# Kernel tuning notes

Hardware: AMD Instinct MI355X
Metric: run time of the kernel (lower is better)

The kernel has to match this reference:

```python
import jax, jax.numpy as jnp
import numpy as np

# MLA dims (DeepSeek-V3-lite style)
B, S, DIM = 1, 2048, 2048
H, NOPE, ROPE, VD, LORA = 16, 128, 64, 128, 512
QK_HEAD = NOPE + ROPE  # 192
SCALE = QK_HEAD ** -0.5
EPS = 1e-6


def _rmsnorm(x, w):
    return x * jax.lax.rsqrt(jnp.mean(x * x, axis=-1, keepdims=True) + EPS) * w


def _apply_rope(x, cos, sin):
    # x: [b, s, h, d] with interleaved (real, imag) pairs; cos/sin: [s, d//2]
    x0, x1 = x[..., 0::2], x[..., 1::2]
    c = cos[None, :, None, :]
    s = sin[None, :, None, :]
    y0 = x0 * c - x1 * s
    y1 = x0 * s + x1 * c
    return jnp.stack([y0, y1], axis=-1).reshape(x.shape)


def setup_inputs() -> dict:
    key = jax.random.key(0)
    ks = jax.random.split(key, 6)
    x = jax.random.normal(ks[0], (B, S, DIM), jnp.float32) * 0.02
    wq = jax.random.normal(ks[1], (H * QK_HEAD, DIM), jnp.float32) * 0.02
    wkv_a = jax.random.normal(ks[2], (LORA + ROPE, DIM), jnp.float32) * 0.02
    kv_norm_w = jnp.ones((LORA,), jnp.float32)
    wkv_b = jax.random.normal(ks[3], (H * (NOPE + VD), LORA), jnp.float32) * 0.02
    wo = jax.random.normal(ks[4], (DIM, H * VD), jnp.float32) * 0.02
    # rotary freqs_cis (cos/sin) for qk_rope_head_dim
    inv_freq = 1.0 / (10000.0 ** (np.arange(0, ROPE, 2, dtype=np.float32) / ROPE))
    t = np.arange(S, dtype=np.float32)
    ang = np.outer(t, inv_freq)  # [S, ROPE//2]
    cos = jnp.asarray(np.cos(ang), jnp.float32)
    sin = jnp.asarray(np.sin(ang), jnp.float32)
    return {"x": x, "cos": cos, "sin": sin, "wq": wq, "wkv_a": wkv_a,
            "kv_norm_w": kv_norm_w, "wkv_b": wkv_b, "wo": wo}


def reference(x, cos, sin, wq, wkv_a, kv_norm_w, wkv_b, wo):
    b, s, _ = x.shape
    # queries
    q = (x @ wq.T).reshape(b, s, H, QK_HEAD)
    q_nope, q_pe = q[..., :NOPE], q[..., NOPE:]
    q_pe = _apply_rope(q_pe, cos, sin)  # [b,s,h,rope]
    # latent kv
    kv = x @ wkv_a.T  # [b,s,lora+rope]
    kv_c, k_pe = kv[..., :LORA], kv[..., LORA:]
    k_pe = _apply_rope(k_pe[:, :, None, :], cos, sin)[:, :, 0, :]  # [b,s,rope]
    kv_c = _rmsnorm(kv_c, kv_norm_w)  # latent kv cache [b,s,lora]
    # absorbed weights: wkv_b viewed as [h, nope+vd, lora]
    wkv_b_r = wkv_b.reshape(H, NOPE + VD, LORA)
    w_uk = wkv_b_r[:, :NOPE]   # [h, nope, lora]
    w_uv = wkv_b_r[:, NOPE:]   # [h, vd, lora]
    # absorb: project q_nope into latent space
    q_c = jnp.einsum('bshd,hdc->bshc', q_nope, w_uk)  # [b,s,h,lora]
    scores = (jnp.einsum('bshc,btc->bsht', q_c, kv_c)
              + jnp.einsum('bshr,btr->bsht', q_pe, k_pe)) * SCALE
    # causal mask over [s, t]
    mask = jnp.where(jnp.arange(s)[:, None] >= jnp.arange(s)[None, :], 0.0, -1e30)
    scores = scores + mask[None, :, None, :].astype(scores.dtype)
    attn = jax.nn.softmax(scores, axis=-1)
    o = jnp.einsum('bsht,btc->bshc', attn, kv_c)       # [b,s,h,lora]
    o = jnp.einsum('bshc,hdc->bshd', o, w_uv)           # [b,s,h,vd]
    out = o.reshape(b, s, H * VD) @ wo.T                # [b,s,dim]
    return out
```

## Files before the change

### kernel.cpp

```cpp
#include <hip/hip_runtime.h>
#include <hip/hip_bf16.h>
#include <math.h>

#define S_LEN 2048
#define DIM   2048
#define H_N   16
#define NOPE  128
#define ROPE  64
#define VD    128
#define LORA  512
#define D_QK  576
#define SCALE_F 0.07216878364870323f
#define EPS_F 1e-6f
#define KVF 640
#define KVS 1280

typedef short short8 __attribute__((ext_vector_type(8)));
typedef short short4v __attribute__((ext_vector_type(4)));
typedef float floatx4 __attribute__((ext_vector_type(4)));

static __device__ inline unsigned short f2bf_bits(float f) {
  union { __hip_bfloat16 h; unsigned short u; } cv;
  cv.h = __float2bfloat16(f);
  return cv.u;
}

static __device__ inline float bf2f(unsigned short b) {
  union { unsigned u; float f; } cv;
  cv.u = (unsigned)b << 16;
  return cv.f;
}

static __device__ inline void gload_lds16(const short* gptr, short* lds_base_uniform) {
  __builtin_amdgcn_global_load_lds(
      (const __attribute__((address_space(1))) void*)gptr,
      (__attribute__((address_space(3))) void*)lds_base_uniform, 16, 0, 0);
}

static __device__ inline void cast8(const float* __restrict__ src,
                                    short* __restrict__ dst, int i) {
  float4 a = ((const float4*)src)[2 * i];
  float4 b = ((const float4*)src)[2 * i + 1];
  uint4 o;
  o.x = (unsigned)f2bf_bits(a.x) | ((unsigned)f2bf_bits(a.y) << 16);
  o.y = (unsigned)f2bf_bits(a.z) | ((unsigned)f2bf_bits(a.w) << 16);
  o.z = (unsigned)f2bf_bits(b.x) | ((unsigned)f2bf_bits(b.y) << 16);
  o.w = (unsigned)f2bf_bits(b.z) | ((unsigned)f2bf_bits(b.w) << 16);
  ((uint4*)dst)[i] = o;
}

#define CSEG0 524288
#define CSEG1 (CSEG0 + 786432)
#define CSEG2 (CSEG1 + 147456)
#define CSEG3 (CSEG2 + 16384)
#define CSEG4 (CSEG3 + 262144)
#define CSEG5 (CSEG4 + 524288)
__global__ __launch_bounds__(256) void cast_all(
    const float* __restrict__ x, const float* __restrict__ wq,
    const float* __restrict__ wkv_a, const float* __restrict__ wkv_b,
    const float* __restrict__ wo, short* __restrict__ xb,
    short* __restrict__ wcat, short* __restrict__ wkvbb,
    short* __restrict__ wob) {
  int i = blockIdx.x * 256 + threadIdx.x;
  if (i < CSEG0) {
    cast8(x, xb, i);
  } else if (i < CSEG1) {
    cast8(wq, wcat, i - CSEG0);
  } else if (i < CSEG2) {
    cast8(wkv_a, wcat + 3072 * 2048, i - CSEG1);
  } else if (i < CSEG3) {
    ((uint4*)(wcat + 3072 * 2048 + 576 * 2048))[i - CSEG2] = (uint4){0u, 0u, 0u, 0u};
  } else if (i < CSEG4) {
    cast8(wkv_b, wkvbb, i - CSEG3);
  } else if (i < CSEG5) {
    cast8(wo, wob, i - CSEG4);
  }
}

__global__ __launch_bounds__(256) void transpose_wuk(
    const float* __restrict__ wkvb, short* __restrict__ wukT) {
  __shared__ float tile[32][33];
  const int h = blockIdx.z, c0 = blockIdx.y * 32, d0 = blockIdx.x * 32;
  const int t = threadIdx.x;
  const int r = t >> 3, c4 = (t & 7) * 4;
  float4 v = *(const float4*)(wkvb + ((long)h * 256 + d0 + r) * 512 + c0 + c4);
  tile[r][c4 + 0] = v.x; tile[r][c4 + 1] = v.y;
  tile[r][c4 + 2] = v.z; tile[r][c4 + 3] = v.w;
  __syncthreads();
  uint2 o;
  o.x = (unsigned)f2bf_bits(tile[c4 + 0][r]) | ((unsigned)f2bf_bits(tile[c4 + 1][r]) << 16);
  o.y = (unsigned)f2bf_bits(tile[c4 + 2][r]) | ((unsigned)f2bf_bits(tile[c4 + 3][r]) << 16);
  *(uint2*)(wukT + ((long)h * 512 + c0 + r) * 128 + d0 + c4) = o;
}

__global__ __launch_bounds__(256) void gemm_bf16_nt_m64(
    const short* __restrict__ A, const short* __restrict__ B, void* __restrict__ Cv,
    int K, int lda, int ldb, int ldc, long aB, long bB, long cB, int bf16out) {
  A += (long)blockIdx.z * aB;
  B += (long)blockIdx.z * bB;
  const int m0 = blockIdx.y * 64, n0 = blockIdx.x * 128;
  __shared__ short As[2][64 * 32];
  __shared__ short Bs[2][128 * 32];
  const int tid = threadIdx.x, w = tid >> 6, lane = tid & 63;
  const int ln = lane & 15, g = lane >> 4;
  const int mw = (w & 1) * 32, nw = (w >> 1) * 64;
  floatx4 acc[2][4];
#pragma unroll
  for (int i = 0; i < 2; ++i)
#pragma unroll
    for (int j = 0; j < 4; ++j) acc[i][j] = (floatx4){0.f, 0.f, 0.f, 0.f};

#define GEMM_STAGE64(k0_, b_)                                                  \
  {                                                                            \
    {                                                                          \
      const int bc = w * 64;                                                   \
      const int c = bc + lane;                                                 \
      const int row = c >> 2, quar = c & 3;                                    \
      gload_lds16(A + (long)(m0 + row) * lda + (k0_) + quar * 8, As[b_] + bc * 8); \
    }                                                                          \
    _Pragma("unroll")                                                          \
    for (int i = 0; i < 2; ++i) {                                              \
      const int bc = (i * 4 + w) * 64;                                         \
      const int c = bc + lane;                                                 \
      const int row = c >> 2, quar = c & 3;                                    \
      gload_lds16(B + (long)(n0 + row) * ldb + (k0_) + quar * 8, Bs[b_] + bc * 8); \
    }                                                                          \
  }

  GEMM_STAGE64(0, 0);
  __syncthreads();
  const int nk = K >> 5;
  for (int kt = 0; kt < nk; ++kt) {
    const int cb = kt & 1;
    if (kt + 1 < nk) GEMM_STAGE64((kt + 1) << 5, cb ^ 1);
    short8 af[2], bf_[4];
#pragma unroll
    for (int mi = 0; mi < 2; ++mi)
      af[mi] = *(const short8*)(As[cb] + (mw + mi * 16 + ln) * 32 + g * 8);
#pragma unroll
    for (int ni = 0; ni < 4; ++ni)
      bf_[ni] = *(const short8*)(Bs[cb] + (nw + ni * 16 + ln) * 32 + g * 8);
#pragma unroll
    for (int mi = 0; mi < 2; ++mi)
#pragma unroll
      for (int ni = 0; ni < 4; ++ni)
        acc[mi][ni] = __builtin_amdgcn_mfma_f32_16x16x32_bf16(af[mi], bf_[ni], acc[mi][ni], 0, 0, 0);
    __syncthreads();
  }
#undef GEMM_STAGE64
  if (bf16out) {
    short* Cs = (short*)Cv + (long)blockIdx.z * cB;
#pragma unroll
    for (int mi = 0; mi < 2; ++mi)
#pragma unroll
      for (int ni = 0; ni < 4; ++ni)
#pragma unroll
        for (int r = 0; r < 4; ++r)
          Cs[(long)(m0 + mw + mi * 16 + g * 4 + r) * ldc + n0 + nw + ni * 16 + ln] =
              (short)f2bf_bits(acc[mi][ni][r]);
  } else {
    float* C = (float*)Cv + (long)blockIdx.z * cB;
#pragma unroll
    for (int mi = 0; mi < 2; ++mi)
#pragma unroll
      for (int ni = 0; ni < 4; ++ni)
#pragma unroll
        for (int r = 0; r < 4; ++r)
          C[(long)(m0 + mw + mi * 16 + g * 4 + r) * ldc + n0 + nw + ni * 16 + ln] = acc[mi][ni][r];
  }
}

__global__ __launch_bounds__(256) void gemm_qkv_m64(
    const short* __restrict__ A, const short* __restrict__ B,
    short* __restrict__ Cq, float* __restrict__ Ckv) {
  const int m0 = blockIdx.y * 64, n0 = blockIdx.x * 128;
  __shared__ short As[2][64 * 32];
  __shared__ short Bs[2][128 * 32];
  const int tid = threadIdx.x, w = tid >> 6, lane = tid & 63;
  const int ln = lane & 15, g = lane >> 4;
  const int mw = (w & 1) * 32, nw = (w >> 1) * 64;
  floatx4 acc[2][4];
#pragma unroll
  for (int i = 0; i < 2; ++i)
#pragma unroll
    for (int j = 0; j < 4; ++j) acc[i][j] = (floatx4){0.f, 0.f, 0.f, 0.f};

#define QKV_STAGE(k0_, b_)                                                     \
  {                                                                            \
    {                                                                          \
      const int bc = w * 64;                                                   \
      const int c = bc + lane;                                                 \
      const int row = c >> 2, quar = c & 3;                                    \
      gload_lds16(A + (long)(m0 + row) * 2048 + (k0_) + quar * 8, As[b_] + bc * 8); \
    }                                                                          \
    _Pragma("unroll")                                                          \
    for (int i = 0; i < 2; ++i) {                                              \
      const int bc = (i * 4 + w) * 64;                                         \
      const int c = bc + lane;                                                 \
      const int row = c >> 2, quar = c & 3;                                    \
      gload_lds16(B + (long)(n0 + row) * 2048 + (k0_) + quar * 8, Bs[b_] + bc * 8); \
    }                                                                          \
  }

  QKV_STAGE(0, 0);
  __syncthreads();
  for (int kt = 0; kt < 64; ++kt) {
    const int cb = kt & 1;
    if (kt + 1 < 64) QKV_STAGE((kt + 1) << 5, cb ^ 1);
    short8 af[2], bf_[4];
#pragma unroll
    for (int mi = 0; mi < 2; ++mi)
      af[mi] = *(const short8*)(As[cb] + (mw + mi * 16 + ln) * 32 + g * 8);
#pragma unroll
    for (int ni = 0; ni < 4; ++ni)
      bf_[ni] = *(const short8*)(Bs[cb] + (nw + ni * 16 + ln) * 32 + g * 8);
#pragma unroll
    for (int mi = 0; mi < 2; ++mi)
#pragma unroll
      for (int ni = 0; ni < 4; ++ni)
        acc[mi][ni] = __builtin_amdgcn_mfma_f32_16x16x32_bf16(af[mi], bf_[ni], acc[mi][ni], 0, 0, 0);
    __syncthreads();
  }
#undef QKV_STAGE
  if (n0 < 3072) {
#pragma unroll
    for (int mi = 0; mi < 2; ++mi)
#pragma unroll
      for (int ni = 0; ni < 4; ++ni)
#pragma unroll
        for (int r = 0; r < 4; ++r)
          Cq[(long)(m0 + mw + mi * 16 + g * 4 + r) * 3072 + n0 + nw + ni * 16 + ln] =
              (short)f2bf_bits(acc[mi][ni][r]);
  } else {
#pragma unroll
    for (int mi = 0; mi < 2; ++mi)
#pragma unroll
      for (int ni = 0; ni < 4; ++ni)
#pragma unroll
        for (int r = 0; r < 4; ++r)
          Ckv[(long)(m0 + mw + mi * 16 + g * 4 + r) * KVF + (n0 - 3072) + nw + ni * 16 + ln] =
              acc[mi][ni][r];
  }
}

__global__ __launch_bounds__(64) void prep_kernel(
    float* kv, const short* __restrict__ qbufb, short* __restrict__ qhatb,
    const float* __restrict__ cosp, const float* __restrict__ sinp,
    const float* __restrict__ normw) {
  const int s = blockIdx.x;
  const int l = threadIdx.x;
  float* row = kv + (long)s * KVF;
  short* krow = (short*)kv + (long)s * KVS;

  float4 v0 = *(const float4*)(row + l * 8);
  float4 v1 = *(const float4*)(row + l * 8 + 4);
  float rx0 = 0.f, rx1 = 0.f, rc = 0.f, rs = 0.f;
  if (l < 32) {
    rc = cosp[s * 32 + l];
    rs = sinp[s * 32 + l];
    rx0 = row[512 + 2 * l];
    rx1 = row[512 + 2 * l + 1];
  }
  float4 w0 = *(const float4*)(normw + l * 8);
  float4 w1 = *(const float4*)(normw + l * 8 + 4);

  float ss = v0.x * v0.x + v0.y * v0.y + v0.z * v0.z + v0.w * v0.w +
             v1.x * v1.x + v1.y * v1.y + v1.z * v1.z + v1.w * v1.w;
#pragma unroll
  for (int off = 32; off; off >>= 1) ss += __shfl_xor(ss, off, 64);
  const float scale = rsqrtf(ss * (1.0f / (float)LORA) + EPS_F);
  v0.x *= scale * w0.x; v0.y *= scale * w0.y; v0.z *= scale * w0.z; v0.w *= scale * w0.w;
  v1.x *= scale * w1.x; v1.y *= scale * w1.y; v1.z *= scale * w1.z; v1.w *= scale * w1.w;

  uint4 pk;
  pk.x = (unsigned)f2bf_bits(v0.x) | ((unsigned)f2bf_bits(v0.y) << 16);
  pk.y = (unsigned)f2bf_bits(v0.z) | ((unsigned)f2bf_bits(v0.w) << 16);
  pk.z = (unsigned)f2bf_bits(v1.x) | ((unsigned)f2bf_bits(v1.y) << 16);
  pk.w = (unsigned)f2bf_bits(v1.z) | ((unsigned)f2bf_bits(v1.w) << 16);
  *(uint4*)(krow + l * 8) = pk;

  if (l < 32) {
    const float y0 = rx0 * rc - rx1 * rs;
    const float y1 = rx0 * rs + rx1 * rc;
    unsigned pr = (unsigned)f2bf_bits(y0) | ((unsigned)f2bf_bits(y1) << 16);
    *(unsigned*)(krow + 512 + 2 * l) = pr;
  }

#pragma unroll
  for (int it = 0; it < 8; ++it) {
    const int p = it * 64 + l;
    const int h = p >> 5;
    const int i = p & 31;
    const float c = cosp[s * 32 + i];
    const float sn = sinp[s * 32 + i];
    const short* qp = qbufb + (long)s * 3072 + h * 192 + NOPE;
    const unsigned uq = *(const unsigned*)(qp + 2 * i);
    const float x0 = bf2f((unsigned short)uq);
    const float x1 = bf2f((unsigned short)(uq >> 16));
    const float y0 = x0 * c - x1 * sn;
    const float y1 = x0 * sn + x1 * c;
    short* dst = qhatb + ((long)h * S_LEN + s) * D_QK + 512;
    *(unsigned*)(dst + 2 * i) = (unsigned)f2bf_bits(y0) | ((unsigned)f2bf_bits(y1) << 16);
  }
}

__global__ __launch_bounds__(256) void transpose_v(
    const short* __restrict__ kbf, short* __restrict__ kvt) {
  __shared__ short tile[32][36];
  const int d0 = blockIdx.x * 32;
  const int s0 = blockIdx.y * 32;
  const int t = threadIdx.x;
  const int r = t >> 3;
  const int c4 = (t & 7) * 4;
  uint2 v = *(const uint2*)(kbf + (long)(s0 + r) * KVS + d0 + c4);
  *(uint2*)(&tile[r][c4]) = v;
  __syncthreads();
  uint2 o;
  o.x = (unsigned)(unsigned short)tile[c4 + 0][r] | ((unsigned)(unsigned short)tile[c4 + 1][r] << 16);
  o.y = (unsigned)(unsigned short)tile[c4 + 2][r] | ((unsigned)(unsigned short)tile[c4 + 3][r] << 16);
  *(uint2*)(kvt + (long)(d0 + r) * S_LEN + s0 + c4) = o;
}

__global__ __launch_bounds__(256) void build_ktt(
    const short* __restrict__ kbf, short* __restrict__ ktt) {
  const int kt = blockIdx.x;
  for (int idx = threadIdx.x; idx < 18 * 64; idx += 256) {
    const int c = idx >> 6, l = idx & 63;
    const int ln = l & 15, g = l >> 4;
    uint4 v = *(const uint4*)(kbf + (long)(kt * 16 + ln) * KVS + c * 32 + g * 8);
    *(uint4*)(ktt + ((long)(kt * 18 + c) * 64 + l) * 8) = v;
  }
}

__global__ __launch_bounds__(256) void build_vtt(
    const short* __restrict__ kvt, short* __restrict__ vtt) {
  const int kt = blockIdx.x;
  for (int idx = threadIdx.x; idx < 32 * 64; idx += 256) {
    const int nt = idx >> 6, l = idx & 63;
    const int ln = l & 15, g = l >> 4;
    uint4 v = *(const uint4*)(kvt + (long)(nt * 16 + ln) * S_LEN + kt * 32 + g * 8);
    *(uint4*)(vtt + ((long)(kt * 32 + nt) * 64 + l) * 8) = v;
  }
}

__global__ __launch_bounds__(512, 2) void flash_reg(
    const short* __restrict__ qhat,
    const short* __restrict__ ktt,
    const short* __restrict__ vtt,
    short* __restrict__ obuf) {
  const int bid = blockIdx.x;
  const int hp = bid & 7;
  const int v = bid >> 3;
  const int vi = v & 31, vj = v >> 5;
  const int qt2 = (vj == 0) ? 63 - vi : vi;
  const int q0 = qt2 * 32;
  const int tid = threadIdx.x;
  const int w = tid >> 6;
  const int lane = tid & 63;
  const int ln = lane & 15, g = lane >> 4;
  const int hh = w & 1;
  const int dh = (w >> 1) & 1;
  const int qt = w >> 2;
  const int h = hp * 2 + hh;
  const int qrow = q0 + qt * 16 + ln;
  const int qlim = qrow;

  __shared__ short Kt[2][36 * 512];
  __shared__ short Vt[2][32 * 512];
  __shared__ __align__(16) short Pl[2][2][2][16][40];
  __shared__ float Ls[8][16];

  short8 qfr[18];
  {
    const short* qr = qhat + ((long)h * S_LEN + qrow) * D_QK;
#pragma unroll
    for (int c = 0; c < 18; ++c)
      qfr[c] = *(const short8*)(qr + c * 32 + g * 8);
  }

  floatx4 oacc[16];
#pragma unroll
  for (int nt = 0; nt < 16; ++nt) oacc[nt] = (floatx4){0.f, 0.f, 0.f, 0.f};
  float lsum = 0.f;

  const int npairs = qt2 + 1;

#define FL_STAGEK(pair_, b_)                                                   \
  {                                                                            \
    const short* ks_ = ktt + (long)(pair_) * (36 * 512);                       \
    _Pragma("unroll")                                                          \
    for (int i = 0; i < 5; ++i) {                                              \
      const int grp = i * 8 + w;                                               \
      if (grp < 36)                                                            \
        gload_lds16(ks_ + (long)(grp * 64 + lane) * 8, Kt[b_] + grp * 512);    \
    }                                                                          \
  }

#define FL_STAGEV(pair_, b_)                                                   \
  {                                                                            \
    const short* vs_ = vtt + (long)(pair_) * (32 * 512);                       \
    _Pragma("unroll")                                                          \
    for (int i = 0; i < 4; ++i) {                                              \
      const int grp = i * 8 + w;                                               \
      gload_lds16(vs_ + (long)(grp * 64 + lane) * 8, Vt[b_] + grp * 512);      \
    }                                                                          \
  }

#define FL_PV(par_)                                                            \
  {                                                                            \
    const short8 pb8 = *(const short8*)(&Pl[par_][hh][qt][ln][g * 8]);         \
    const short* vb_ = Vt[par_] + dh * (16 * 512);                             \
    _Pragma("unroll")                                                          \
    for (int half = 0; half < 2; ++half) {                                     \
      short8 va[8];                                                            \
      _Pragma("unroll")                                                        \
      for (int j = 0; j < 8; ++j)                                              \
        va[j] = *(const short8*)(vb_ + (half * 8 + j) * 512 + lane * 8);       \
      __builtin_amdgcn_s_setprio(1);                                           \
      _Pragma("unroll")                                                        \
      for (int j = 0; j < 8; ++j)                                              \
        oacc[half * 8 + j] = __builtin_amdgcn_mfma_f32_16x16x32_bf16(          \
            va[j], pb8, oacc[half * 8 + j], 0, 0, 0);                          \
      __builtin_amdgcn_s_setprio(0);                                           \
    }                                                                          \
  }

  FL_STAGEK(0, 0);
  __syncthreads();

  for (int p = 0; p < npairs; ++p) {
    const int cb = p & 1;
    if (p + 1 < npairs) FL_STAGEK(p + 1, cb ^ 1);
    FL_STAGEV(p, cb);
    const short* kb = Kt[cb] + dh * (18 * 512);
    floatx4 s0 = (floatx4){0.f, 0.f, 0.f, 0.f};
    floatx4 s1 = (floatx4){0.f, 0.f, 0.f, 0.f};
    __builtin_amdgcn_s_setprio(1);
#pragma unroll
    for (int c = 0; c < 18; c += 2) {
      short8 k0 = *(const short8*)(kb + (c * 64 + lane) * 8);
      short8 k1 = *(const short8*)(kb + ((c + 1) * 64 + lane) * 8);
      s0 = __builtin_amdgcn_mfma_f32_16x16x32_bf16(k0, qfr[c], s0, 0, 0, 0);
      s1 = __builtin_amdgcn_mfma_f32_16x16x32_bf16(k1, qfr[c + 1], s1, 0, 0, 0);
    }
    __builtin_amdgcn_s_setprio(0);
    short4v p4;
    float psum = 0.f;
#pragma unroll
    for (int r = 0; r < 4; ++r) {
      const int ki = p * 32 + dh * 16 + g * 4 + r;
      float sc = fminf(fmaxf((s0[r] + s1[r]) * SCALE_F, -30.f), 30.f);
      float pv_ = (ki <= qlim) ? __expf(sc) : 0.f;
      psum += pv_;
      p4[r] = (short)f2bf_bits(pv_);
    }
    lsum += psum;
    union { short4v s; unsigned long long u; } upk;
    upk.s = p4;
    *(unsigned long long*)(&Pl[cb][hh][qt][ln][dh * 16 + g * 4]) = upk.u;
    if (p > 0) FL_PV(cb ^ 1);
    __syncthreads();
  }
  FL_PV((npairs - 1) & 1);
#undef FL_PV
#undef FL_STAGEV
#undef FL_STAGEK

  lsum += __shfl_xor(lsum, 16, 64);
  lsum += __shfl_xor(lsum, 32, 64);
  if (g == 0) Ls[w][ln] = lsum;
  __syncthreads();
  lsum += Ls[w ^ 2][ln];
  const float inv = 1.0f / fmaxf(lsum, 1e-30f);

  short* orow = obuf + ((long)h * S_LEN + qrow) * 512 + dh * 256 + g * 4;
#pragma unroll
  for (int nt = 0; nt < 16; ++nt) {
    unsigned lo = (unsigned)f2bf_bits(oacc[nt][0] * inv) | ((unsigned)f2bf_bits(oacc[nt][1] * inv) << 16);
    unsigned hi = (unsigned)f2bf_bits(oacc[nt][2] * inv) | ((unsigned)f2bf_bits(oacc[nt][3] * inv) << 16);
    unsigned long long st = (unsigned long long)lo | ((unsigned long long)hi << 32);
    *(unsigned long long*)(orow + nt * 16) = st;
  }
}

extern "C" void kernel_launch(void* const* d_in, const int* in_sizes, int n_in,
                              void* d_out, int out_size, void* d_ws, size_t ws_size,
                              hipStream_t stream) {
  (void)in_sizes; (void)n_in; (void)out_size; (void)ws_size;
  const float* x      = (const float*)d_in[0];
  const float* cosp   = (const float*)d_in[1];
  const float* sinp   = (const float*)d_in[2];
  const float* wq     = (const float*)d_in[3];
  const float* wkv_a  = (const float*)d_in[4];
  const float* normw  = (const float*)d_in[5];
  const float* wkv_b  = (const float*)d_in[6];
  const float* wo     = (const float*)d_in[7];
  float* out = (float*)d_out;

  float* ws = (float*)d_ws;
  float* qbufR  = ws;
  float* kvold  = qbufR + (long)S_LEN * 3072;
  float* qhatR  = kvold + (long)S_LEN * D_QK;
  float* obufR  = qhatR + (long)H_N * S_LEN * D_QK;
  float* oprojR = obufR + (long)H_N * S_LEN * LORA;

  float* kvpad = oprojR;
  short* kbf = (short*)kvpad;

  short* qbufb = (short*)qbufR;
  short* kvt = qbufb + (long)S_LEN * 3072;
  short* ktt = kvt + (long)512 * S_LEN;
  short* vtt = ktt + (long)128 * 18 * 64 * 8;

  short* qhatb  = (short*)qhatR;
  short* wkvbb  = qhatb + (long)H_N * S_LEN * D_QK;
  short* oprojb = wkvbb + (long)4096 * 512;
  short* wob    = oprojb + (long)2048 * 2048;

  short* xb   = (short*)obufR;
  short* wcat = xb + (long)2048 * 2048;
  short* wukT = wcat + (long)3712 * 2048;
  short* obufb = (short*)obufR;

  cast_all<<<dim3(CSEG5 / 256), 256, 0, stream>>>(
      x, wq, wkv_a, wkv_b, wo, xb, wcat, wkvbb, wob);

  gemm_qkv_m64<<<dim3(3712 / 128, 2048 / 64, 1), 256, 0, stream>>>(
      xb, wcat, qbufb, kvpad);

  prep_kernel<<<dim3(S_LEN), 64, 0, stream>>>(kvpad, qbufb, qhatb, cosp, sinp, normw);

  transpose_wuk<<<dim3(4, 16, 16), 256, 0, stream>>>(wkv_b, wukT);

  gemm_bf16_nt_m64<<<dim3(512 / 128, 2048 / 64, 16), 256, 0, stream>>>(
      qbufb, wukT, qhatb, 128, 3072, 128, 576,
      192L, 512L * 128, (long)S_LEN * D_QK, 1);

  transpose_v<<<dim3(16, 64), 256, 0, stream>>>(kbf, kvt);
  build_ktt<<<dim3(128), 256, 0, stream>>>(kbf, ktt);
  build_vtt<<<dim3(64), 256, 0, stream>>>(kvt, vtt);

  flash_reg<<<dim3(512), 512, 0, stream>>>(qhatb, ktt, vtt, obufb);

  gemm_bf16_nt_m64<<<dim3(1, 2048 / 64, 16), 256, 0, stream>>>(
      obufb, wkvbb + 128L * 512, oprojb, 512, 512, 512, 2048,
      (long)S_LEN * 512, 256L * 512, 128L, 1);

  gemm_bf16_nt_m64<<<dim3(2048 / 128, 2048 / 64, 1), 256, 0, stream>>>(
      oprojb, wob, out, 2048, 2048, 2048, 2048, 0, 0, 0, 0);
}
```

Baseline: 404.4 us.

## Fuse W_uv up-projection into flash attention epilogue

The flash attention kernel now stages its normalized latent output tile in shared memory (reusing the K buffer) and multiplies it by the W_uv slice with MFMA inside the same kernel. It writes the per-head value projection directly into the o_proj buffer. This removes the separate batched GEMM launch and the 16x2048x512 bf16 round trip of the latent attention output through global memory. In exchange the attention kernel gains an epilogue that reads W_uv from global memory per block, with no staging or reuse, and adds an extra barrier.

```diff
diff --git a/kernel.cpp b/kernel.cpp
--- a/kernel.cpp
+++ b/kernel.cpp
@@ -347,7 +347,8 @@
     const short* __restrict__ qhat,
     const short* __restrict__ ktt,
     const short* __restrict__ vtt,
-    short* __restrict__ obuf) {
+    const short* __restrict__ wuv,
+    short* __restrict__ oproj) {
   const int bid = blockIdx.x;
   const int hp = bid & 7;
   const int v = bid >> 3;
@@ -473,13 +474,42 @@
   lsum += Ls[w ^ 2][ln];
   const float inv = 1.0f / fmaxf(lsum, 1e-30f);
 
-  short* orow = obuf + ((long)h * S_LEN + qrow) * 512 + dh * 256 + g * 4;
-#pragma unroll
-  for (int nt = 0; nt < 16; ++nt) {
-    unsigned lo = (unsigned)f2bf_bits(oacc[nt][0] * inv) | ((unsigned)f2bf_bits(oacc[nt][1] * inv) << 16);
-    unsigned hi = (unsigned)f2bf_bits(oacc[nt][2] * inv) | ((unsigned)f2bf_bits(oacc[nt][3] * inv) << 16);
-    unsigned long long st = (unsigned long long)lo | ((unsigned long long)hi << 32);
-    *(unsigned long long*)(orow + nt * 16) = st;
+  short* Ob = &Kt[0][0];
+  {
+    short* obr = Ob + ((hh * 32 + qt * 16 + ln) * 520) + dh * 256 + g * 4;
+#pragma unroll
+    for (int nt = 0; nt < 16; ++nt) {
+      unsigned lo = (unsigned)f2bf_bits(oacc[nt][0] * inv) | ((unsigned)f2bf_bits(oacc[nt][1] * inv) << 16);
+      unsigned hi = (unsigned)f2bf_bits(oacc[nt][2] * inv) | ((unsigned)f2bf_bits(oacc[nt][3] * inv) << 16);
+      unsigned long long st = (unsigned long long)lo | ((unsigned long long)hi << 32);
+      *(unsigned long long*)(obr + nt * 16) = st;
+    }
+  }
+  __syncthreads();
+
+  {
+    const short* wuvb = wuv + ((long)(h * 256 + 128 + dh * 64)) * 512;
+    const short* obq = Ob + (hh * 32 + qt * 16 + ln) * 520;
+    floatx4 pacc[4];
+#pragma unroll
+    for (int dt = 0; dt < 4; ++dt) pacc[dt] = (floatx4){0.f, 0.f, 0.f, 0.f};
+#pragma unroll 4
+    for (int ks = 0; ks < 16; ++ks) {
+      short8 bfr = *(const short8*)(obq + ks * 32 + g * 8);
+#pragma unroll
+      for (int dt = 0; dt < 4; ++dt) {
+        short8 afr = *(const short8*)(wuvb + ((long)(dt * 16 + ln)) * 512 + ks * 32 + g * 8);
+        pacc[dt] = __builtin_amdgcn_mfma_f32_16x16x32_bf16(afr, bfr, pacc[dt], 0, 0, 0);
+      }
+    }
+    short* orow = oproj + ((long)qrow) * 2048 + h * 128 + dh * 64 + g * 4;
+#pragma unroll
+    for (int dt = 0; dt < 4; ++dt) {
+      unsigned lo = (unsigned)f2bf_bits(pacc[dt][0]) | ((unsigned)f2bf_bits(pacc[dt][1]) << 16);
+      unsigned hi = (unsigned)f2bf_bits(pacc[dt][2]) | ((unsigned)f2bf_bits(pacc[dt][3]) << 16);
+      unsigned long long st = (unsigned long long)lo | ((unsigned long long)hi << 32);
+      *(unsigned long long*)(orow + dt * 16) = st;
+    }
   }
 }
 
@@ -520,7 +550,6 @@
   short* xb   = (short*)obufR;
   short* wcat = xb + (long)2048 * 2048;
   short* wukT = wcat + (long)3712 * 2048;
-  short* obufb = (short*)obufR;
 
   cast_all<<<dim3(CSEG5 / 256), 256, 0, stream>>>(
       x, wq, wkv_a, wkv_b, wo, xb, wcat, wkvbb, wob);
@@ -540,11 +569,7 @@
   build_ktt<<<dim3(128), 256, 0, stream>>>(kbf, ktt);
   build_vtt<<<dim3(64), 256, 0, stream>>>(kvt, vtt);
 
-  flash_reg<<<dim3(512), 512, 0, stream>>>(qhatb, ktt, vtt, obufb);
-
-  gemm_bf16_nt_m64<<<dim3(1, 2048 / 64, 16), 256, 0, stream>>>(
-      obufb, wkvbb + 128L * 512, oprojb, 512, 512, 512, 2048,
-      (long)S_LEN * 512, 256L * 512, 128L, 1);
+  flash_reg<<<dim3(512), 512, 0, stream>>>(qhatb, ktt, vtt, wkvbb, oprojb);
 
   gemm_bf16_nt_m64<<<dim3(2048 / 128, 2048 / 64, 1), 256, 0, stream>>>(
       oprojb, wob, out, 2048, 2048, 2048, 2048, 0, 0, 0, 0);
```

Measured after the change: 413.7 us. 2.3% more time.
